# Kernel tuning notes

Hardware: AMD Instinct MI355X
Metric: run time of the kernel (lower is better)

Reference implementation:

```python
import jax, jax.numpy as jnp
import numpy as np

B, M, N = 32, 1024, 1024

def setup_inputs() -> dict:
    key = jax.random.key(0)
    ks = jax.random.split(key, 7)
    return {
        "pred_r": jax.random.normal(ks[0], (B, M, 4), jnp.float32),
        "pred_t": jax.random.normal(ks[1], (B, M, 3), jnp.float32),
        "pred_c": jax.random.uniform(ks[2], (B, M), jnp.float32),
        "target": jax.random.normal(ks[3], (B, N, 3), jnp.float32),
        "model_points": jax.random.normal(ks[4], (B, N, 3), jnp.float32),
        "idx": jax.random.randint(ks[5], (B,), 0, 21),
        "points": jax.random.normal(ks[6], (B, M, 3), jnp.float32),
        "w": jnp.float32(0.015),
        "refine": 1,
    }

def quat_to_rotmat(q):
    # q: (B, M, 4) in xyzw order -> R: (B, M, 3, 3)
    q = q / (jnp.linalg.norm(q, axis=2, keepdims=True) + 1e-8)
    qx, qy, qz, qw = q[..., 0], q[..., 1], q[..., 2], q[..., 3]
    r1 = jnp.stack([1 - 2 * (qy * qy + qz * qz), 2 * (qx * qy - qz * qw), 2 * (qx * qz + qy * qw)], axis=-1)
    r2 = jnp.stack([2 * (qx * qy + qz * qw), 1 - 2 * (qx * qx + qz * qz), 2 * (qy * qz - qx * qw)], axis=-1)
    r3 = jnp.stack([2 * (qx * qz - qy * qw), 2 * (qy * qz + qx * qw), 1 - 2 * (qx * qx + qy * qy)], axis=-1)
    return jnp.stack([r1, r2, r3], axis=-2)

def reference(pred_r, pred_t, pred_c, target, model_points, idx, points, w, refine):
    # refine=True path (no symmetric-object KNN correspondence); idx/sym_list unused.
    pred_c = jnp.maximum(pred_c, 1e-6)                          # (B, M)
    R = quat_to_rotmat(pred_r)                                  # (B, M, 3, 3)
    # row-vector transform: mpR[b,m,n,j] = sum_i model_points[b,n,i] * R[b,m,i,j]
    mpR = jnp.einsum('bni,bmij->bmnj', model_points, R)         # (B, M, N, 3)
    pred_xyz = mpR + (points + pred_t)[:, :, None, :]           # (B, M, N, 3)
    diff = pred_xyz - target[:, None, :, :]
    dis_h = jnp.sqrt(jnp.sum(diff * diff, axis=-1)).mean(axis=2)  # (B, M)
    loss = jnp.mean(dis_h * pred_c - w * jnp.log(pred_c))
    which_max = jnp.argmax(pred_c, axis=1)                      # (B,)
    bidx = jnp.arange(B)
    R_best = R[bidx, which_max]                                 # (B, 3, 3)
    t_best = (points + pred_t)[bidx, which_max][:, None, :]     # (B, 1, 3)
    new_points = jnp.einsum('bmi,bij->bmj', points - t_best, R_best)
    new_target = jnp.einsum('bni,bij->bnj', target - t_best, R_best)
    dis_best = dis_h[bidx, which_max].mean()
    return (loss, dis_best,
            jax.lax.stop_gradient(new_points),
            jax.lax.stop_gradient(new_target))
```

## Files before the change

### kernel.cpp

```cpp
#include <hip/hip_runtime.h>

#define Bn 32
#define Mn 1024
#define Nn 1024

__device__ __forceinline__ void quat_to_R(float qx, float qy, float qz, float qw,
                                          float R[9]) {
    float norm = sqrtf(qx*qx + qy*qy + qz*qz + qw*qw) + 1e-8f;
    float inv = 1.0f / norm;
    float x = qx*inv, y = qy*inv, z = qz*inv, w = qw*inv;
    R[0] = 1.0f - 2.0f*(y*y + z*z);
    R[1] = 2.0f*(x*y - z*w);
    R[2] = 2.0f*(x*z + y*w);
    R[3] = 2.0f*(x*y + z*w);
    R[4] = 1.0f - 2.0f*(x*x + z*z);
    R[5] = 2.0f*(y*z - x*w);
    R[6] = 2.0f*(x*z - y*w);
    R[7] = 2.0f*(y*z + x*w);
    R[8] = 1.0f - 2.0f*(x*x + y*y);
}

__global__ __launch_bounds__(256) void k1_dis_loss(
    const float* __restrict__ pred_r, const float* __restrict__ pred_t,
    const float* __restrict__ pred_c, const float* __restrict__ target,
    const float* __restrict__ model_points, const float* __restrict__ points,
    const float* __restrict__ wptr, float* __restrict__ loss_accum)
{
    __shared__ __align__(16) float s[Nn * 8];
    __shared__ float red[256];

    const int b    = blockIdx.x >> 4;
    const int mc   = blockIdx.x & 15;
    const int tid  = threadIdx.x;
    const int lane = tid & 63;
    const int ng   = tid >> 6;

    const float* mp_flat = model_points + b * Nn * 3;
    const float* tg_flat = target      + b * Nn * 3;
    for (int i = tid; i < Nn * 3; i += 256) {
        int n = i / 3;
        int r = i - n * 3;
        s[n * 8 + r]     = mp_flat[i];
        s[n * 8 + 3 + r] = tg_flat[i];
    }

    const int gm = b * Mn + mc * 64 + lane;
    float4 q = *(const float4*)(pred_r + gm * 4);
    float R[9];
    quat_to_R(q.x, q.y, q.z, q.w, R);
    const float tx = points[gm*3+0] + pred_t[gm*3+0];
    const float ty = points[gm*3+1] + pred_t[gm*3+1];
    const float tz = points[gm*3+2] + pred_t[gm*3+2];

    __syncthreads();

    float ssum = 0.0f;
    const int n0 = ng * 256;
    #pragma unroll 4
    for (int n = n0; n < n0 + 256; ++n) {
        const float* row = s + n * 8;
        float4 a  = *(const float4*)(row);
        float2 c2 = *(const float2*)(row + 4);
        float px = fmaf(a.x, R[0], fmaf(a.y, R[3], fmaf(a.z, R[6], tx)));
        float py = fmaf(a.x, R[1], fmaf(a.y, R[4], fmaf(a.z, R[7], ty)));
        float pz = fmaf(a.x, R[2], fmaf(a.y, R[5], fmaf(a.z, R[8], tz)));
        float dx = px - a.w;
        float dy = py - c2.x;
        float dz = pz - c2.y;
        ssum += sqrtf(fmaf(dx, dx, fmaf(dy, dy, dz * dz)));
    }

    red[tid] = ssum;
    __syncthreads();

    if (ng == 0) {
        float tot = red[lane] + red[lane + 64] + red[lane + 128] + red[lane + 192];
        float dis = tot * (1.0f / (float)Nn);
        float c = fmaxf(pred_c[gm], 1e-6f);
        float w = *wptr;
        float contrib = fmaf(dis, c, -w * logf(c));
        for (int off = 32; off > 0; off >>= 1)
            contrib += __shfl_down(contrib, off);
        if (lane == 0)
            atomicAdd(loss_accum, contrib);
    }
}

__global__ __launch_bounds__(256) void k2_best(
    const float* __restrict__ pred_r, const float* __restrict__ pred_t,
    const float* __restrict__ pred_c, const float* __restrict__ target,
    const float* __restrict__ model_points, const float* __restrict__ points,
    const float* __restrict__ loss_accum, float* __restrict__ out)
{
    const int b   = blockIdx.x;
    const int tid = threadIdx.x;

    __shared__ float sv[256];
    __shared__ int   si[256];
    __shared__ float Rt[12];
    __shared__ float wred[4];

    float bv = -1e30f; int bi = Mn;
    for (int m = tid; m < Mn; m += 256) {
        float v = pred_c[b * Mn + m];
        if (v > bv) { bv = v; bi = m; }
    }
    sv[tid] = bv; si[tid] = bi;
    __syncthreads();
    for (int off = 128; off > 0; off >>= 1) {
        if (tid < off) {
            float v2 = sv[tid + off]; int i2 = si[tid + off];
            if (v2 > sv[tid] || (v2 == sv[tid] && i2 < si[tid])) {
                sv[tid] = v2; si[tid] = i2;
            }
        }
        __syncthreads();
    }

    if (tid == 0) {
        int m = si[0];
        int gm = b * Mn + m;
        float4 q = *(const float4*)(pred_r + gm * 4);
        float R[9];
        quat_to_R(q.x, q.y, q.z, q.w, R);
        #pragma unroll
        for (int i = 0; i < 9; ++i) Rt[i] = R[i];
        Rt[9]  = points[gm*3+0] + pred_t[gm*3+0];
        Rt[10] = points[gm*3+1] + pred_t[gm*3+1];
        Rt[11] = points[gm*3+2] + pred_t[gm*3+2];
    }
    __syncthreads();

    const float R0 = Rt[0], R1 = Rt[1], R2 = Rt[2];
    const float R3 = Rt[3], R4 = Rt[4], R5 = Rt[5];
    const float R6 = Rt[6], R7 = Rt[7], R8 = Rt[8];
    const float tx = Rt[9], ty = Rt[10], tz = Rt[11];

    float ssum = 0.0f;
    for (int n = tid; n < Nn; n += 256) {
        const float* mp = model_points + (b * Nn + n) * 3;
        const float* tg = target      + (b * Nn + n) * 3;
        float px = fmaf(mp[0], R0, fmaf(mp[1], R3, fmaf(mp[2], R6, tx)));
        float py = fmaf(mp[0], R1, fmaf(mp[1], R4, fmaf(mp[2], R7, ty)));
        float pz = fmaf(mp[0], R2, fmaf(mp[1], R5, fmaf(mp[2], R8, tz)));
        float dx = px - tg[0], dy = py - tg[1], dz = pz - tg[2];
        ssum += sqrtf(fmaf(dx, dx, fmaf(dy, dy, dz * dz)));
    }
    for (int off = 32; off > 0; off >>= 1)
        ssum += __shfl_down(ssum, off);
    if ((tid & 63) == 0) wred[tid >> 6] = ssum;
    __syncthreads();
    if (tid == 0) {
        float tot = wred[0] + wred[1] + wred[2] + wred[3];
        atomicAdd(out + 1, tot * (1.0f / (float)Nn) * (1.0f / (float)Bn));
        if (b == 0)
            out[0] = loss_accum[0] * (1.0f / ((float)Bn * (float)Mn));
    }

    float* np_out = out + 2;
    float* nt_out = out + 2 + Bn * Mn * 3;
    for (int m = tid; m < Mn; m += 256) {
        const float* p = points + (b * Mn + m) * 3;
        float x = p[0] - tx, y = p[1] - ty, z = p[2] - tz;
        float* o = np_out + (b * Mn + m) * 3;
        o[0] = fmaf(x, R0, fmaf(y, R3, z * R6));
        o[1] = fmaf(x, R1, fmaf(y, R4, z * R7));
        o[2] = fmaf(x, R2, fmaf(y, R5, z * R8));
    }
    for (int n = tid; n < Nn; n += 256) {
        const float* p = target + (b * Nn + n) * 3;
        float x = p[0] - tx, y = p[1] - ty, z = p[2] - tz;
        float* o = nt_out + (b * Nn + n) * 3;
        o[0] = fmaf(x, R0, fmaf(y, R3, z * R6));
        o[1] = fmaf(x, R1, fmaf(y, R4, z * R7));
        o[2] = fmaf(x, R2, fmaf(y, R5, z * R8));
    }
}

extern "C" void kernel_launch(void* const* d_in, const int* in_sizes, int n_in,
                              void* d_out, int out_size, void* d_ws, size_t ws_size,
                              hipStream_t stream) {
    const float* pred_r       = (const float*)d_in[0];
    const float* pred_t       = (const float*)d_in[1];
    const float* pred_c       = (const float*)d_in[2];
    const float* target       = (const float*)d_in[3];
    const float* model_points = (const float*)d_in[4];
    const float* points       = (const float*)d_in[6];
    const float* wptr         = (const float*)d_in[7];

    float* out        = (float*)d_out;
    float* loss_accum = (float*)d_ws;

    hipMemsetAsync(loss_accum, 0, sizeof(float), stream);
    hipMemsetAsync(out, 0, 2 * sizeof(float), stream);

    k1_dis_loss<<<Bn * (Mn / 64), 256, 0, stream>>>(
        pred_r, pred_t, pred_c, target, model_points, points, wptr, loss_accum);
    k2_best<<<Bn, 256, 0, stream>>>(
        pred_r, pred_t, pred_c, target, model_points, points, loss_accum, out);
}
```

Baseline: 113.0 us.

## Drop memsets, fuse argmax into loss kernel, widen finalize grid

The per-block argmax of pred_c and the per-block loss partial are now computed in the first kernel and written to workspace instead of going through an atomic, which removes both hipMemsetAsync calls. The second kernel now reduces those partials and runs 8 blocks per batch rather than 1 to parallelise the output transforms and the dis_best sum. sqrtf is replaced by the raw hardware sqrt builtin in the inner loop. This trades launch overhead and serial tail work for reliance on the first kernel zeroing out[1] before the second kernel's atomics, and a slightly less precise sqrt.

Result: faster. 98.98 us (-12.4%).

```diff
diff --git a/kernel.cpp b/kernel.cpp
--- a/kernel.cpp
+++ b/kernel.cpp
@@ -4,9 +4,11 @@
 #define Mn 1024
 #define Nn 1024
 
+__device__ __forceinline__ float fsqrt(float x) { return __builtin_amdgcn_sqrtf(x); }
+
 __device__ __forceinline__ void quat_to_R(float qx, float qy, float qz, float qw,
                                           float R[9]) {
-    float norm = sqrtf(qx*qx + qy*qy + qz*qz + qw*qw) + 1e-8f;
+    float norm = fsqrt(qx*qx + qy*qy + qz*qz + qw*qw) + 1e-8f;
     float inv = 1.0f / norm;
     float x = qx*inv, y = qy*inv, z = qz*inv, w = qw*inv;
     R[0] = 1.0f - 2.0f*(y*y + z*z);
@@ -24,7 +26,11 @@
     const float* __restrict__ pred_r, const float* __restrict__ pred_t,
     const float* __restrict__ pred_c, const float* __restrict__ target,
     const float* __restrict__ model_points, const float* __restrict__ points,
-    const float* __restrict__ wptr, float* __restrict__ loss_accum)
+    const float* __restrict__ wptr,
+    float* __restrict__ ws_loss,
+    float* __restrict__ ws_amax,
+    int*   __restrict__ ws_aidx,
+    float* __restrict__ out)
 {
     __shared__ __align__(16) float s[Nn * 8];
     __shared__ float red[256];
@@ -34,6 +40,8 @@
     const int tid  = threadIdx.x;
     const int lane = tid & 63;
     const int ng   = tid >> 6;
+
+    if (blockIdx.x == 0 && tid == 0) out[1] = 0.0f;
 
     const float* mp_flat = model_points + b * Nn * 3;
     const float* tg_flat = target      + b * Nn * 3;
@@ -67,7 +75,7 @@
         float dx = px - a.w;
         float dy = py - c2.x;
         float dz = pz - c2.y;
-        ssum += sqrtf(fmaf(dx, dx, fmaf(dy, dy, dz * dz)));
+        ssum += fsqrt(fmaf(dx, dx, fmaf(dy, dy, dz * dz)));
     }
 
     red[tid] = ssum;
@@ -79,101 +87,102 @@
         float c = fmaxf(pred_c[gm], 1e-6f);
         float w = *wptr;
         float contrib = fmaf(dis, c, -w * logf(c));
+
+        float av = c;
+        int   ai = mc * 64 + lane;
+        #pragma unroll
+        for (int off = 32; off > 0; off >>= 1) {
+            float ov = __shfl_xor(av, off);
+            int   oi = __shfl_xor(ai, off);
+            if (ov > av || (ov == av && oi < ai)) { av = ov; ai = oi; }
+        }
+        #pragma unroll
         for (int off = 32; off > 0; off >>= 1)
             contrib += __shfl_down(contrib, off);
-        if (lane == 0)
-            atomicAdd(loss_accum, contrib);
-    }
-}
-
-__global__ __launch_bounds__(256) void k2_best(
+
+        if (lane == 0) {
+            ws_loss[blockIdx.x] = contrib;
+            ws_amax[blockIdx.x] = av;
+            ws_aidx[blockIdx.x] = ai;
+        }
+    }
+}
+
+__global__ __launch_bounds__(256) void k2_finalize(
     const float* __restrict__ pred_r, const float* __restrict__ pred_t,
-    const float* __restrict__ pred_c, const float* __restrict__ target,
-    const float* __restrict__ model_points, const float* __restrict__ points,
-    const float* __restrict__ loss_accum, float* __restrict__ out)
+    const float* __restrict__ target, const float* __restrict__ model_points,
+    const float* __restrict__ points,
+    const float* __restrict__ ws_loss, const float* __restrict__ ws_amax,
+    const int* __restrict__ ws_aidx,
+    float* __restrict__ out)
 {
-    const int b   = blockIdx.x;
+    const int b   = blockIdx.x >> 3;
+    const int sl  = blockIdx.x & 7;
     const int tid = threadIdx.x;
 
-    __shared__ float sv[256];
-    __shared__ int   si[256];
-    __shared__ float Rt[12];
-    __shared__ float wred[4];
-
-    float bv = -1e30f; int bi = Mn;
-    for (int m = tid; m < Mn; m += 256) {
-        float v = pred_c[b * Mn + m];
-        if (v > bv) { bv = v; bi = m; }
-    }
-    sv[tid] = bv; si[tid] = bi;
-    __syncthreads();
-    for (int off = 128; off > 0; off >>= 1) {
-        if (tid < off) {
-            float v2 = sv[tid + off]; int i2 = si[tid + off];
-            if (v2 > sv[tid] || (v2 == sv[tid] && i2 < si[tid])) {
-                sv[tid] = v2; si[tid] = i2;
-            }
-        }
-        __syncthreads();
-    }
-
-    if (tid == 0) {
-        int m = si[0];
-        int gm = b * Mn + m;
-        float4 q = *(const float4*)(pred_r + gm * 4);
-        float R[9];
-        quat_to_R(q.x, q.y, q.z, q.w, R);
-        #pragma unroll
-        for (int i = 0; i < 9; ++i) Rt[i] = R[i];
-        Rt[9]  = points[gm*3+0] + pred_t[gm*3+0];
-        Rt[10] = points[gm*3+1] + pred_t[gm*3+1];
-        Rt[11] = points[gm*3+2] + pred_t[gm*3+2];
-    }
-    __syncthreads();
-
-    const float R0 = Rt[0], R1 = Rt[1], R2 = Rt[2];
-    const float R3 = Rt[3], R4 = Rt[4], R5 = Rt[5];
-    const float R6 = Rt[6], R7 = Rt[7], R8 = Rt[8];
-    const float tx = Rt[9], ty = Rt[10], tz = Rt[11];
+    __shared__ float wredA[4];
+    __shared__ float wredB[4];
+
+    float bv = -1.0f; int bi = Mn;
+    #pragma unroll
+    for (int k = 0; k < 16; ++k) {
+        float v = ws_amax[b * 16 + k];
+        int   i = ws_aidx[b * 16 + k];
+        if (v > bv || (v == bv && i < bi)) { bv = v; bi = i; }
+    }
+    const int gm = b * Mn + bi;
+    float4 q = *(const float4*)(pred_r + gm * 4);
+    float R[9];
+    quat_to_R(q.x, q.y, q.z, q.w, R);
+    const float tx = points[gm*3+0] + pred_t[gm*3+0];
+    const float ty = points[gm*3+1] + pred_t[gm*3+1];
+    const float tz = points[gm*3+2] + pred_t[gm*3+2];
+
+    {
+        const int t   = tid & 127;
+        const int idx = sl * 128 + t;
+        const bool is_p = (tid < 128);
+        const float* src = is_p ? (points + (b * Mn + idx) * 3)
+                                : (target + (b * Nn + idx) * 3);
+        float* dst = is_p ? (out + 2 + (b * Mn + idx) * 3)
+                          : (out + 2 + Bn * Mn * 3 + (b * Nn + idx) * 3);
+        float x = src[0] - tx, y = src[1] - ty, z = src[2] - tz;
+        dst[0] = fmaf(x, R[0], fmaf(y, R[3], z * R[6]));
+        dst[1] = fmaf(x, R[1], fmaf(y, R[4], z * R[7]));
+        dst[2] = fmaf(x, R[2], fmaf(y, R[5], z * R[8]));
+    }
 
     float ssum = 0.0f;
-    for (int n = tid; n < Nn; n += 256) {
+    if (tid < 128) {
+        const int n = sl * 128 + tid;
         const float* mp = model_points + (b * Nn + n) * 3;
         const float* tg = target      + (b * Nn + n) * 3;
-        float px = fmaf(mp[0], R0, fmaf(mp[1], R3, fmaf(mp[2], R6, tx)));
-        float py = fmaf(mp[0], R1, fmaf(mp[1], R4, fmaf(mp[2], R7, ty)));
-        float pz = fmaf(mp[0], R2, fmaf(mp[1], R5, fmaf(mp[2], R8, tz)));
+        float px = fmaf(mp[0], R[0], fmaf(mp[1], R[3], fmaf(mp[2], R[6], tx)));
+        float py = fmaf(mp[0], R[1], fmaf(mp[1], R[4], fmaf(mp[2], R[7], ty)));
+        float pz = fmaf(mp[0], R[2], fmaf(mp[1], R[5], fmaf(mp[2], R[8], tz)));
         float dx = px - tg[0], dy = py - tg[1], dz = pz - tg[2];
-        ssum += sqrtf(fmaf(dx, dx, fmaf(dy, dy, dz * dz)));
-    }
+        ssum = fsqrt(fmaf(dx, dx, fmaf(dy, dy, dz * dz)));
+    }
+    #pragma unroll
     for (int off = 32; off > 0; off >>= 1)
         ssum += __shfl_down(ssum, off);
-    if ((tid & 63) == 0) wred[tid >> 6] = ssum;
+    if ((tid & 63) == 0) wredA[tid >> 6] = ssum;
     __syncthreads();
     if (tid == 0) {
-        float tot = wred[0] + wred[1] + wred[2] + wred[3];
-        atomicAdd(out + 1, tot * (1.0f / (float)Nn) * (1.0f / (float)Bn));
-        if (b == 0)
-            out[0] = loss_accum[0] * (1.0f / ((float)Bn * (float)Mn));
-    }
-
-    float* np_out = out + 2;
-    float* nt_out = out + 2 + Bn * Mn * 3;
-    for (int m = tid; m < Mn; m += 256) {
-        const float* p = points + (b * Mn + m) * 3;
-        float x = p[0] - tx, y = p[1] - ty, z = p[2] - tz;
-        float* o = np_out + (b * Mn + m) * 3;
-        o[0] = fmaf(x, R0, fmaf(y, R3, z * R6));
-        o[1] = fmaf(x, R1, fmaf(y, R4, z * R7));
-        o[2] = fmaf(x, R2, fmaf(y, R5, z * R8));
-    }
-    for (int n = tid; n < Nn; n += 256) {
-        const float* p = target + (b * Nn + n) * 3;
-        float x = p[0] - tx, y = p[1] - ty, z = p[2] - tz;
-        float* o = nt_out + (b * Nn + n) * 3;
-        o[0] = fmaf(x, R0, fmaf(y, R3, z * R6));
-        o[1] = fmaf(x, R1, fmaf(y, R4, z * R7));
-        o[2] = fmaf(x, R2, fmaf(y, R5, z * R8));
+        float tot = wredA[0] + wredA[1] + wredA[2] + wredA[3];
+        atomicAdd(out + 1, tot * (1.0f / ((float)Nn * (float)Bn)));
+    }
+
+    if (blockIdx.x == 0) {
+        float ls = ws_loss[tid] + ws_loss[tid + 256];
+        #pragma unroll
+        for (int off = 32; off > 0; off >>= 1)
+            ls += __shfl_down(ls, off);
+        if ((tid & 63) == 0) wredB[tid >> 6] = ls;
+        __syncthreads();
+        if (tid == 0)
+            out[0] = (wredB[0] + wredB[1] + wredB[2] + wredB[3])
+                     * (1.0f / ((float)Bn * (float)Mn));
     }
 }
 
@@ -188,14 +197,15 @@
     const float* points       = (const float*)d_in[6];
     const float* wptr         = (const float*)d_in[7];
 
-    float* out        = (float*)d_out;
-    float* loss_accum = (float*)d_ws;
-
-    hipMemsetAsync(loss_accum, 0, sizeof(float), stream);
-    hipMemsetAsync(out, 0, 2 * sizeof(float), stream);
+    float* out     = (float*)d_out;
+    float* ws_loss = (float*)d_ws;
+    float* ws_amax = ws_loss + 512;
+    int*   ws_aidx = (int*)(ws_loss + 1024);
 
     k1_dis_loss<<<Bn * (Mn / 64), 256, 0, stream>>>(
-        pred_r, pred_t, pred_c, target, model_points, points, wptr, loss_accum);
-    k2_best<<<Bn, 256, 0, stream>>>(
-        pred_r, pred_t, pred_c, target, model_points, points, loss_accum, out);
-}
+        pred_r, pred_t, pred_c, target, model_points, points, wptr,
+        ws_loss, ws_amax, ws_aidx, out);
+    k2_finalize<<<8 * Bn, 256, 0, stream>>>(
+        pred_r, pred_t, target, model_points, points,
+        ws_loss, ws_amax, ws_aidx, out);
+}
```
